# Optimization experiments

Measured on AMD Instinct MI355X. Metric: run time of the kernel, lower is better.

## Reference

```python
import jax, jax.numpy as jnp
import numpy as np

B, S, D, H, E, K = 4, 2048, 1024, 4096, 8, 2
CAP = 2048      # expert capacity (tokens)
ALPHA = 0.01    # load-balance loss coefficient


def setup_inputs() -> dict:
    key = jax.random.key(0)
    ks = jax.random.split(key, 8)
    def w(k, shape, fan_in):
        return jax.random.normal(k, shape, jnp.float32) * (fan_in ** -0.5)
    return {
        "input": jax.random.normal(ks[0], (B, S, D), jnp.float32),
        "rw": w(ks[1], (D, E), D), "rb": jnp.zeros((E,), jnp.float32),
        "w1": w(ks[2], (E, D, H), D), "b1": jnp.zeros((E, H), jnp.float32),
        "w2": w(ks[3], (E, H, D), H), "b2": jnp.zeros((E, D), jnp.float32),
        "ow1": w(ks[4], (D, H), D), "ob1": jnp.zeros((H,), jnp.float32),
        "ow2": w(ks[5], (H, D), H), "ob2": jnp.zeros((D,), jnp.float32),
    }


def _moe(x, rw, rb, w1, b1, w2, b2, ow1, ob1, ow2, ob2):
    Bx, Sx, Dx = x.shape
    N = Bx * Sx
    xf = x.reshape(N, Dx)

    # --- router: softmax -> top-k -> renormalize ---
    scores = jax.nn.softmax(xf @ rw + rb, axis=-1)          # [N,E]
    tw, ti = jax.lax.top_k(scores, K)                       # [N,K]
    tw = tw / tw.sum(-1, keepdims=True)
    onehot = jax.nn.one_hot(ti, E, dtype=xf.dtype)          # [N,K,E]
    w_ne = jnp.einsum('nk,nke->ne', tw, onehot)             # combine weight per (token, expert)
    mask = onehot.sum(1) > 0                                # [N,E]
    mi = mask.astype(jnp.int32)

    # exclusive rank of each token within its expert's queue (token order, as torch nonzero())
    rank = jnp.cumsum(mi, axis=0) - mi                      # [N,E]
    within = mask & (rank < CAP)
    over = mask & (rank >= CAP)

    # --- dispatch within-capacity tokens into [E, CAP] slots (sentinel = N) ---
    tok = jnp.broadcast_to(jnp.arange(N, dtype=jnp.int32)[:, None], (N, E))
    eid = jnp.broadcast_to(jnp.arange(E, dtype=jnp.int32)[None, :], (N, E))
    slot = jnp.where(within, rank, CAP)                     # non-assigned -> pad column
    buf = jnp.full((E, CAP + 1), N, dtype=jnp.int32)
    buf = buf.at[eid.reshape(-1), slot.reshape(-1)].set(tok.reshape(-1))
    buf = buf[:, :CAP]                                      # [E,CAP]

    xpad = jnp.concatenate([xf, jnp.zeros((1, Dx), xf.dtype)], axis=0)
    xd = xpad[buf]                                          # [E,CAP,D]

    # --- grouped expert FFN (Linear -> relu -> Linear) ---
    h = jax.nn.relu(jnp.einsum('ecd,edh->ech', xd, w1) + b1[:, None, :])
    y = jnp.einsum('ech,ehd->ecd', h, w2) + b2[:, None, :]  # [E,CAP,D]

    # combine weights gathered per slot; pad slots get weight 0
    wpad = jnp.concatenate([w_ne, jnp.zeros((1, E), w_ne.dtype)], axis=0)
    wc = wpad[buf, jnp.arange(E, dtype=jnp.int32)[:, None]]  # [E,CAP]

    outpad = jnp.zeros((N + 1, Dx), xf.dtype)
    outpad = outpad.at[buf.reshape(-1)].add((wc[..., None] * y).reshape(-1, Dx))
    out = outpad[:N]

    # --- overflow tokens -> shared overflow FFN (computed densely, masked by weight) ---
    w_of = (w_ne * over.astype(w_ne.dtype)).sum(-1)          # [N]
    yo = jax.nn.relu(xf @ ow1 + ob1) @ ow2 + ob2             # [N,D]
    out = out + w_of[:, None] * yo

    # --- aux load-balance loss (detached in torch via .item()) ---
    num = mi.sum(0)                                          # [E]
    cnt = jnp.minimum(num, CAP)
    f = cnt.astype(xf.dtype) / N
    p = (w_ne * within.astype(w_ne.dtype)).sum(0) / jnp.maximum(cnt, 1).astype(xf.dtype)
    aux = ALPHA * E * jnp.sum(f * p)
    return out.reshape(Bx, Sx, Dx), jax.lax.stop_gradient(aux)


def reference(input, rw, rb, w1, b1, w2, b2, ow1, ob1, ow2, ob2):
    return _moe(input, rw, rb, w1, b1, w2, b2, ow1, ob1, ow2, ob2)
```

## Files before the change

kernel.cpp:

```cpp
#include <hip/hip_runtime.h>
#include <cstdint>

typedef __attribute__((ext_vector_type(8))) short bf16x8;
typedef __attribute__((ext_vector_type(4))) float f32x4;

#define N_TOK    8192
#define DMODEL   1024
#define HDIM     4096
#define CAPACITY 2048

__device__ __forceinline__ unsigned short f2bf(float f) {
  unsigned u = __float_as_uint(f);
  u += 0x7FFFu + ((u >> 16) & 1u);
  return (unsigned short)(u >> 16);
}

__device__ __forceinline__ void gl_lds16(const unsigned short* g, unsigned short* l) {
  __builtin_amdgcn_global_load_lds(
      (const __attribute__((address_space(1))) void*)g,
      (__attribute__((address_space(3))) void*)l, 16, 0, 0);
}

__global__ void cvtx_kernel(const float* __restrict__ x, unsigned short* __restrict__ xb) {
  long i0 = ((long)blockIdx.x * 256 + threadIdx.x) * 16;
#pragma unroll
  for (int ii = 0; ii < 4; ii++) {
    float4 v = *(const float4*)(x + i0 + ii * 4);
    ushort4 u;
    u.x = f2bf(v.x); u.y = f2bf(v.y); u.z = f2bf(v.z); u.w = f2bf(v.w);
    *(ushort4*)(xb + i0 + ii * 4) = u;
  }
}

__global__ void router_kernel(const float* __restrict__ x, const float* __restrict__ rw,
                              const float* __restrict__ rb, int4* __restrict__ recs) {
  int wave = threadIdx.x >> 6;
  int lane = threadIdx.x & 63;
  int tok = blockIdx.x * 4 + wave;
  const float* xr = x + (long)tok * DMODEL;
  float s[8];
#pragma unroll
  for (int e = 0; e < 8; e++) s[e] = 0.f;
  for (int ii = 0; ii < DMODEL / 64; ii++) {
    int k = lane + 64 * ii;
    float xv = xr[k];
    const float* wr = rw + k * 8;
    float4 a = *(const float4*)wr;
    float4 b = *(const float4*)(wr + 4);
    s[0] += xv * a.x; s[1] += xv * a.y; s[2] += xv * a.z; s[3] += xv * a.w;
    s[4] += xv * b.x; s[5] += xv * b.y; s[6] += xv * b.z; s[7] += xv * b.w;
  }
#pragma unroll
  for (int m = 1; m < 64; m <<= 1) {
#pragma unroll
    for (int e = 0; e < 8; e++) s[e] += __shfl_xor(s[e], m);
  }
  if (lane == 0) {
#pragma unroll
    for (int e = 0; e < 8; e++) s[e] += rb[e];
    int b0 = 0; float v0 = s[0];
#pragma unroll
    for (int e = 1; e < 8; e++) if (s[e] > v0) { v0 = s[e]; b0 = e; }
    int b1 = -1; float v1 = 0.f;
#pragma unroll
    for (int e = 0; e < 8; e++) {
      if (e == b0) continue;
      if (b1 < 0 || s[e] > v1) { v1 = s[e]; b1 = e; }
    }
    float t0 = 1.f / (1.f + expf(v1 - v0));
    float t1 = 1.f - t0;
    recs[tok] = make_int4(b0, b1, __float_as_int(t0), __float_as_int(t1));
  }
}

__device__ __forceinline__ int bump16(uint4& v, int e) {
  unsigned sh = (e & 1) ? 16u : 0u;
  unsigned inc = 1u << sh;
  unsigned old;
  switch (e >> 1) {
    case 0: old = v.x; v.x += inc; break;
    case 1: old = v.y; v.y += inc; break;
    case 2: old = v.z; v.z += inc; break;
    default: old = v.w; v.w += inc; break;
  }
  return (int)((old >> sh) & 0xFFFFu);
}

__device__ __forceinline__ unsigned field16(uint4 v, int e) {
  unsigned w;
  switch (e >> 1) { case 0: w = v.x; break; case 1: w = v.y; break; case 2: w = v.z; break; default: w = v.w; break; }
  return (w >> ((e & 1) ? 16 : 0)) & 0xFFFFu;
}

__global__ void assign_kernel(const int4* __restrict__ recs, int* __restrict__ buf,
                              float* __restrict__ wc, int* __restrict__ cnt,
                              float* __restrict__ auxOut) {
  __shared__ uint4 sc[1024];
  __shared__ unsigned sco[1024];
  __shared__ float pnum[8];
  int tid = threadIdx.x;
  if (tid < 8) pnum[tid] = 0.f;
  int4 rc[8];
#pragma unroll
  for (int i = 0; i < 8; i++) {
    rc[i] = recs[tid * 8 + i];
    rc[i].x &= 7; rc[i].y &= 7;
  }
  uint4 c; c.x = c.y = c.z = c.w = 0u;
#pragma unroll
  for (int i = 0; i < 8; i++) { bump16(c, rc[i].x); bump16(c, rc[i].y); }
  sc[tid] = c;
  __syncthreads();
  for (int off = 1; off < 1024; off <<= 1) {
    uint4 v; v.x = v.y = v.z = v.w = 0u;
    if (tid >= off) v = sc[tid - off];
    __syncthreads();
    sc[tid].x += v.x; sc[tid].y += v.y; sc[tid].z += v.z; sc[tid].w += v.w;
    __syncthreads();
  }
  uint4 base; base.x = base.y = base.z = base.w = 0u;
  if (tid > 0) base = sc[tid - 1];
  uint4 totals = sc[1023];

  uint4 run = base;
  float wof[8];
  unsigned oc = 0;
#pragma unroll
  for (int i = 0; i < 8; i++) {
    int tk = tid * 8 + i;
    int e0 = rc[i].x, e1 = rc[i].y;
    float w0 = __int_as_float(rc[i].z);
    float w1 = __int_as_float(rc[i].w);
    float w = 0.f;
    int r0 = bump16(run, e0);
    if (r0 < CAPACITY) {
      buf[e0 * CAPACITY + r0] = tk;
      wc[e0 * CAPACITY + r0] = w0;
      atomicAdd(&pnum[e0], w0);
    } else w += w0;
    int r1 = bump16(run, e1);
    if (r1 < CAPACITY) {
      buf[e1 * CAPACITY + r1] = tk;
      wc[e1 * CAPACITY + r1] = w1;
      atomicAdd(&pnum[e1], w1);
    } else w += w1;
    wof[i] = w;
    if (w > 0.f) oc++;
  }
  sco[tid] = oc;
  __syncthreads();
  for (int off = 1; off < 1024; off <<= 1) {
    unsigned v = (tid >= off) ? sco[tid - off] : 0u;
    __syncthreads();
    sco[tid] += v;
    __syncthreads();
  }
  unsigned ob = (tid > 0) ? sco[tid - 1] : 0u;
  unsigned Ot = sco[1023];
#pragma unroll
  for (int i = 0; i < 8; i++) {
    if (wof[i] > 0.f) {
      unsigned slot = ob++;
      int ve = 8 + (int)(slot >> 11);
      buf[ve * CAPACITY + (int)(slot & 2047)] = tid * 8 + i;
      wc[ve * CAPACITY + (int)(slot & 2047)] = wof[i];
    }
  }
  __syncthreads();
  if (tid == 0) {
    float aux = 0.f;
#pragma unroll
    for (int e = 0; e < 8; e++) {
      int tot = (int)field16(totals, e);
      int c2 = tot < CAPACITY ? tot : CAPACITY;
      cnt[e] = c2;
      float f = (float)c2 / (float)N_TOK;
      float p = pnum[e] / (float)(c2 > 1 ? c2 : 1);
      aux += f * p;
    }
#pragma unroll
    for (int i = 0; i < 4; i++) {
      int c2 = (int)Ot - i * CAPACITY;
      c2 = c2 < 0 ? 0 : (c2 > CAPACITY ? CAPACITY : c2);
      cnt[8 + i] = c2;
    }
    auxOut[0] = 0.01f * 8.f * aux;
  }
}

__global__ __launch_bounds__(256) void transpose_all(
    const float* __restrict__ w1, const float* __restrict__ w2,
    const float* __restrict__ ow1, const float* __restrict__ ow2,
    unsigned short* __restrict__ wt1, unsigned short* __restrict__ wt2,
    long slotStride, int pairBase) {
  int pair = pairBase + blockIdx.x / 2048;
  int t = blockIdx.x & 2047;
  long srcOff = (long)pair * DMODEL * HDIM;
  long dstOff = (long)(blockIdx.x / 2048) * slotStride;
  const float* in; unsigned short* out; int R, C;
  if (t < 1024) {
    in = (pair < 8) ? w1 + srcOff : ow1;
    out = wt1 + dstOff;
    R = DMODEL; C = HDIM;
  } else {
    in = (pair < 8) ? w2 + srcOff : ow2;
    out = wt2 + dstOff;
    R = HDIM; C = DMODEL;
    t -= 1024;
  }
  int tr = t / (C >> 6);
  int tc = t % (C >> 6);
  int r0 = tr << 6, c0 = tc << 6;
  __shared__ float tl[64][65];
  int row = threadIdx.x >> 4, cg = threadIdx.x & 15;
#pragma unroll
  for (int i = 0; i < 4; i++) {
    int r = row + 16 * i;
    float4 v = *(const float4*)(in + (long)(r0 + r) * C + c0 + cg * 4);
    tl[r][cg * 4 + 0] = v.x; tl[r][cg * 4 + 1] = v.y;
    tl[r][cg * 4 + 2] = v.z; tl[r][cg * 4 + 3] = v.w;
  }
  __syncthreads();
#pragma unroll
  for (int i = 0; i < 4; i++) {
    int oc = row + 16 * i;
    ushort4 o;
    o.x = f2bf(tl[cg * 4 + 0][oc]);
    o.y = f2bf(tl[cg * 4 + 1][oc]);
    o.z = f2bf(tl[cg * 4 + 2][oc]);
    o.w = f2bf(tl[cg * 4 + 3][oc]);
    *(ushort4*)(out + (long)(c0 + oc) * R + r0 + cg * 4) = o;
  }
}


#define STAGE_A(Ab, kk)                                             \
  { _Pragma("unroll") for (int s = 0; s < 4; s++)                   \
      gl_lds16(asrc[s] + (kk), &(Ab)[wave * 2048 + s * 512]); }
#define STAGE_B(Bb, kk)                                             \
  { _Pragma("unroll") for (int s = 0; s < 4; s++)                   \
      gl_lds16(bsrc[s] + (kk), &(Bb)[wave * 2048 + s * 512]); }

#define R_A_FRAGS(dst, Abuf, ks)                                               \
  { _Pragma("unroll") for (int mi = 0; mi < 8; mi++) {                         \
      int r = mo + mi * 16 + l15;                                              \
      dst[mi] = *(const bf16x8*)&(Abuf)[r * 64 + ((((ks) * 4 + hi) ^ (r & 7)) << 3)]; \
    } }
#define R_B_FRAGS(dst, Bbuf, ks)                                               \
  { _Pragma("unroll") for (int ni = 0; ni < 4; ni++) {                         \
      int r = no + ni * 16 + l15;                                              \
      dst[ni] = *(const bf16x8*)&(Bbuf)[r * 64 + ((((ks) * 4 + hi) ^ (r & 7)) << 3)]; \
    } }

#define MFMA32(fa, fb)                                                         \
  { __builtin_amdgcn_s_setprio(1);                                             \
    _Pragma("unroll") for (int mi = 0; mi < 8; mi++)                           \
      _Pragma("unroll") for (int ni = 0; ni < 4; ni++)                         \
        acc[mi][ni] = __builtin_amdgcn_mfma_f32_16x16x32_bf16(fa[mi], fb[ni], acc[mi][ni], 0, 0, 0); \
    __builtin_amdgcn_s_setprio(0); }

#define K_PIPELINE(NT)                                              \
  do {                                                              \
    STAGE_A(As[0], 0); STAGE_B(Bs[0], 0);                           \
    STAGE_A(As[1], 64); STAGE_B(Bs[1], 64);                         \
    for (int t = 0; t < (NT); t++) {                                \
      unsigned short* Ac = As[t & 1];                               \
      unsigned short* Bc = Bs[t & 1];                               \
      if (t + 1 < (NT)) { asm volatile("s_waitcnt vmcnt(8)"); }     \
      else              { asm volatile("s_waitcnt vmcnt(0)"); }     \
      __builtin_amdgcn_sched_barrier(0);                            \
      __builtin_amdgcn_s_barrier();                                 \
      __builtin_amdgcn_sched_barrier(0);                            \
      bf16x8 fa0[8], fa1[8], fb0[4], fb1[4];                        \
      R_A_FRAGS(fa0, Ac, 0);                                        \
      R_A_FRAGS(fa1, Ac, 1);                                        \
      R_B_FRAGS(fb0, Bc, 0);                                        \
      __builtin_amdgcn_s_barrier();                                 \
      __builtin_amdgcn_sched_barrier(0);                            \
      if (t + 2 < (NT)) STAGE_A(Ac, (t + 2) * 64);                  \
      MFMA32(fa0, fb0);                                             \
      R_B_FRAGS(fb1, Bc, 1);                                        \
      __builtin_amdgcn_s_barrier();                                 \
      __builtin_amdgcn_sched_barrier(0);                            \
      if (t + 2 < (NT)) STAGE_B(Bc, (t + 2) * 64);                  \
      MFMA32(fa1, fb1);                                             \
    }                                                               \
  } while (0)

__global__ __launch_bounds__(512, 2) void gemm1_kernel(
    const unsigned short* __restrict__ xb, const int* __restrict__ buf,
    const int* __restrict__ cnt, const unsigned short* __restrict__ wt1, long wtStride,
    const float* __restrict__ b1, const float* __restrict__ ob1,
    unsigned short* __restrict__ h, long hStride, int eBase,
    const unsigned short* __restrict__ zp) {
  int q = gridDim.x >> 3;
  int bx = blockIdx.x;
  int id = (bx & 7) * q + (bx >> 3);
  int e = eBase + id / 128;
  int rem = id % 128;
  int mb = rem >> 4, nb = rem & 15;
  int m0 = mb * 256, n0 = nb * 256;
  if (m0 >= cnt[e]) return;
  const int* bufe = buf + e * CAPACITY;
  int slot = e < 8 ? e : 8;
  const unsigned short* wte = wt1 + (long)slot * wtStride;
  const float* bias = (e < 8) ? b1 + (long)e * HDIM : ob1;
  unsigned short* he = h + (long)e * hStride;

  __shared__ unsigned short As[2][256 * 64];
  __shared__ unsigned short Bs[2][256 * 64];

  int tid = threadIdx.x;
  int wave = tid >> 6, lane = tid & 63;
  int l15 = lane & 15, hi = lane >> 4;
  int wr = wave >> 2, wcv = wave & 3;
  int mo = wr * 128, no = wcv * 64;

  int rlo = lane >> 3;
  int cg = (lane & 7) ^ rlo;
  const unsigned short* asrc[4];
  const unsigned short* bsrc[4];
#pragma unroll
  for (int s = 0; s < 4; s++) {
    int r = wave * 32 + s * 8 + rlo;
    int tok = bufe[m0 + r];
    asrc[s] = ((unsigned)tok < (unsigned)N_TOK) ? (xb + (long)tok * DMODEL + cg * 8)
                                                : (zp + cg * 8);
    bsrc[s] = wte + (long)(n0 + r) * DMODEL + cg * 8;
  }

  f32x4 zero4 = {0.f, 0.f, 0.f, 0.f};
  f32x4 acc[8][4];
#pragma unroll
  for (int mi = 0; mi < 8; mi++)
#pragma unroll
    for (int ni = 0; ni < 4; ni++) acc[mi][ni] = zero4;

  K_PIPELINE(DMODEL / 64);

#pragma unroll
  for (int ni = 0; ni < 4; ni++) {
    int col = n0 + no + ni * 16 + l15;
    float bv = bias[col];
#pragma unroll
    for (int mi = 0; mi < 8; mi++) {
#pragma unroll
      for (int j = 0; j < 4; j++) {
        int mr = m0 + mo + mi * 16 + hi * 4 + j;
        float val = acc[mi][ni][j] + bv;
        val = val > 0.f ? val : 0.f;
        he[(long)mr * HDIM + col] = f2bf(val);
      }
    }
  }
}

__global__ __launch_bounds__(512, 2) void gemm2_kernel(
    const unsigned short* __restrict__ h, long hStride,
    const unsigned short* __restrict__ wt2, long wtStride,
    const float* __restrict__ b2, const float* __restrict__ ob2,
    const int* __restrict__ buf, const float* __restrict__ wc,
    const int* __restrict__ cnt, float* __restrict__ out,
    int eBase, int per, int klen) {
  int q = gridDim.x >> 3;
  int bx = blockIdx.x;
  int id = (bx & 7) * q + (bx >> 3);
  int e = eBase + id / per;
  int rem = id % per;
  int tile = rem & 31;
  int kc = rem >> 5;
  int mb = tile >> 2, nb = tile & 3;
  int m0 = mb * 256, n0 = nb * 256;
  if (m0 >= cnt[e]) return;
  const int* bufe = buf + e * CAPACITY;
  const float* wce = wc + e * CAPACITY;
  int slot = e < 8 ? e : 8;
  const unsigned short* wte = wt2 + (long)slot * wtStride;
  const float* bias = (e < 8) ? b2 + (long)e * DMODEL : ob2;
  const unsigned short* he = h + (long)e * hStride;
  int kbase = kc * klen;

  __shared__ unsigned short As[2][256 * 64];
  __shared__ unsigned short Bs[2][256 * 64];

  int tid = threadIdx.x;
  int wave = tid >> 6, lane = tid & 63;
  int l15 = lane & 15, hi = lane >> 4;
  int wr = wave >> 2, wcv = wave & 3;
  int mo = wr * 128, no = wcv * 64;

  int rlo = lane >> 3;
  int cg = (lane & 7) ^ rlo;
  const unsigned short* asrc[4];
  const unsigned short* bsrc[4];
#pragma unroll
  for (int s = 0; s < 4; s++) {
    int r = wave * 32 + s * 8 + rlo;
    asrc[s] = he + (long)(m0 + r) * HDIM + kbase + cg * 8;
    bsrc[s] = wte + (long)(n0 + r) * HDIM + kbase + cg * 8;
  }

  f32x4 zero4 = {0.f, 0.f, 0.f, 0.f};
  f32x4 acc[8][4];
#pragma unroll
  for (int mi = 0; mi < 8; mi++)
#pragma unroll
    for (int ni = 0; ni < 4; ni++) acc[mi][ni] = zero4;

  K_PIPELINE(klen / 64);

  float bcol[4];
#pragma unroll
  for (int ni = 0; ni < 4; ni++)
    bcol[ni] = (kc == 0) ? bias[n0 + no + ni * 16 + l15] : 0.f;
#pragma unroll
  for (int mi = 0; mi < 8; mi++) {
#pragma unroll
    for (int j = 0; j < 4; j++) {
      int m = m0 + mo + mi * 16 + hi * 4 + j;
      int t = bufe[m];
      if ((unsigned)t >= (unsigned)N_TOK) continue;
      float wv = wce[m];
      float* orow = out + (long)t * DMODEL;
#pragma unroll
      for (int ni = 0; ni < 4; ni++) {
        int col = n0 + no + ni * 16 + l15;
        float val = wv * (acc[mi][ni][j] + bcol[ni]);
        atomicAdd(orow + col, val);
      }
    }
  }
}

extern "C" void kernel_launch(void* const* d_in, const int* in_sizes, int n_in,
                              void* d_out, int out_size, void* d_ws, size_t ws_size,
                              hipStream_t stream) {
  const float* x   = (const float*)d_in[0];
  const float* rw  = (const float*)d_in[1];
  const float* rb  = (const float*)d_in[2];
  const float* w1  = (const float*)d_in[3];
  const float* b1  = (const float*)d_in[4];
  const float* w2  = (const float*)d_in[5];
  const float* b2  = (const float*)d_in[6];
  const float* ow1 = (const float*)d_in[7];
  const float* ob1 = (const float*)d_in[8];
  const float* ow2 = (const float*)d_in[9];
  const float* ob2 = (const float*)d_in[10];
  float* out = (float*)d_out;

  const long WSLOT = (long)DMODEL * HDIM;
  const long HSLOT = (long)CAPACITY * HDIM;

  bool fused = ws_size >= 380ull * 1024 * 1024;

  char* ws = (char*)d_ws;
  int4* recs = (int4*)(ws);
  int*  buf  = (int*)(ws + 131072);
  float* wcp = (float*)(ws + 229376);
  int*  cnt  = (int*)(ws + 327680);
  unsigned short* zp = (unsigned short*)(ws + 331776);
  unsigned short* xb  = (unsigned short*)(ws + 1048576);
  unsigned short* wt1 = (unsigned short*)(ws + 17825792);
  unsigned short* wt2;
  unsigned short* h;
  if (fused) {
    wt2 = (unsigned short*)(ws + 93323264);
    h   = (unsigned short*)(ws + 168820736);
  } else {
    wt2 = (unsigned short*)(ws + 26214400);
    h   = (unsigned short*)(ws + 34603008);
  }

  hipMemsetAsync(d_out, 0, (size_t)out_size * sizeof(float), stream);
  hipMemsetAsync(buf, 0xFF, 12 * CAPACITY * sizeof(int), stream);
  hipMemsetAsync(wcp, 0, 12 * CAPACITY * sizeof(float), stream);
  hipMemsetAsync(zp, 0, 2048, stream);

  cvtx_kernel<<<2048, 256, 0, stream>>>(x, xb);
  router_kernel<<<2048, 256, 0, stream>>>(x, rw, rb, recs);
  assign_kernel<<<1, 1024, 0, stream>>>(recs, buf, wcp, cnt, out + (long)N_TOK * DMODEL);

  if (fused) {
    transpose_all<<<9 * 2048, 256, 0, stream>>>(w1, w2, ow1, ow2, wt1, wt2, WSLOT, 0);
    gemm1_kernel<<<12 * 128, 512, 0, stream>>>(xb, buf, cnt, wt1, WSLOT, b1, ob1, h, HSLOT, 0, zp);
    gemm2_kernel<<<12 * 64, 512, 0, stream>>>(h, HSLOT, wt2, WSLOT, b2, ob2, buf, wcp, cnt, out,
                                              0, 64, HDIM / 2);
  } else {
    for (int e = 0; e < 12; e++) {
      if (e <= 8)
        transpose_all<<<2048, 256, 0, stream>>>(w1, w2, ow1, ow2, wt1, wt2, 0, e);
      gemm1_kernel<<<128, 512, 0, stream>>>(xb, buf, cnt, wt1, 0, b1, ob1, h, 0, e, zp);
      gemm2_kernel<<<64, 512, 0, stream>>>(h, 0, wt2, 0, b2, ob2, buf, wcp, cnt, out,
                                           e, 64, HDIM / 2);
    }
  }
}
```

Baseline: 660.3 us.

## Replace atomic scatter-add in down-proj with bf16 partials plus per-token reduce

```diff
diff --git a/kernel.cpp b/kernel.cpp
--- a/kernel.cpp
+++ b/kernel.cpp
@@ -8,11 +8,15 @@
 #define DMODEL   1024
 #define HDIM     4096
 #define CAPACITY 2048
+#define YKC      (12L * CAPACITY * DMODEL)
 
 __device__ __forceinline__ unsigned short f2bf(float f) {
   unsigned u = __float_as_uint(f);
   u += 0x7FFFu + ((u >> 16) & 1u);
   return (unsigned short)(u >> 16);
+}
+__device__ __forceinline__ float bf2f(unsigned short s) {
+  return __uint_as_float((unsigned)s << 16);
 }
 
 __device__ __forceinline__ void gl_lds16(const unsigned short* g, unsigned short* l) {
@@ -94,7 +98,7 @@
 
 __global__ void assign_kernel(const int4* __restrict__ recs, int* __restrict__ buf,
                               float* __restrict__ wc, int* __restrict__ cnt,
-                              float* __restrict__ auxOut) {
+                              int* __restrict__ trec, float* __restrict__ auxOut) {
   __shared__ uint4 sc[1024];
   __shared__ unsigned sco[1024];
   __shared__ float pnum[8];
@@ -144,6 +148,12 @@
       wc[e1 * CAPACITY + r1] = w1;
       atomicAdd(&pnum[e1], w1);
     } else w += w1;
+    trec[tk * 8 + 0] = (r0 < CAPACITY) ? (e0 * CAPACITY + r0) : -1;
+    trec[tk * 8 + 1] = (r1 < CAPACITY) ? (e1 * CAPACITY + r1) : -1;
+    trec[tk * 8 + 2] = -1;
+    trec[tk * 8 + 4] = rc[i].z;
+    trec[tk * 8 + 5] = rc[i].w;
+    trec[tk * 8 + 6] = 0;
     wof[i] = w;
     if (w > 0.f) oc++;
   }
@@ -162,8 +172,11 @@
     if (wof[i] > 0.f) {
       unsigned slot = ob++;
       int ve = 8 + (int)(slot >> 11);
-      buf[ve * CAPACITY + (int)(slot & 2047)] = tid * 8 + i;
+      int tk = tid * 8 + i;
+      buf[ve * CAPACITY + (int)(slot & 2047)] = tk;
       wc[ve * CAPACITY + (int)(slot & 2047)] = wof[i];
+      trec[tk * 8 + 2] = ve * CAPACITY + (int)(slot & 2047);
+      trec[tk * 8 + 6] = __float_as_int(wof[i]);
     }
   }
   __syncthreads();
@@ -287,6 +300,34 @@
     }                                                               \
   } while (0)
 
+#define EPILOGUE(VALEXPR, DSTPTR, DSTSTRIDE)                                   \
+  do {                                                                         \
+    __syncthreads();                                                           \
+    unsigned short* EP = &As[0][0];                                            \
+    for (int p = 0; p < 2; p++) {                                              \
+      if (wr == p) {                                                           \
+        _Pragma("unroll") for (int mi = 0; mi < 8; mi++) {                     \
+          _Pragma("unroll") for (int ni = 0; ni < 4; ni++) {                   \
+            int col = no + ni * 16 + l15;                                      \
+            _Pragma("unroll") for (int j = 0; j < 4; j++) {                    \
+              int row = mi * 16 + hi * 4 + j;                                  \
+              float v = (VALEXPR);                                             \
+              EP[row * 256 + (col ^ ((row & 7) << 3))] = f2bf(v);              \
+            }                                                                  \
+          }                                                                    \
+        }                                                                      \
+      }                                                                        \
+      __syncthreads();                                                         \
+      _Pragma("unroll") for (int k = 0; k < 8; k++) {                          \
+        int c = tid + 512 * k;                                                 \
+        int row = c >> 5, cc = c & 31;                                         \
+        uint4 v = *(const uint4*)&EP[row * 256 + ((cc ^ (row & 7)) << 3)];     \
+        *(uint4*)&(DSTPTR)[(long)(m0 + p * 128 + row) * (DSTSTRIDE) + n0 + cc * 8] = v; \
+      }                                                                        \
+      __syncthreads();                                                         \
+    }                                                                          \
+  } while (0)
+
 __global__ __launch_bounds__(512, 2) void gemm1_kernel(
     const unsigned short* __restrict__ xb, const int* __restrict__ buf,
     const int* __restrict__ cnt, const unsigned short* __restrict__ wt1, long wtStride,
@@ -338,24 +379,104 @@
 
   K_PIPELINE(DMODEL / 64);
 
-#pragma unroll
-  for (int ni = 0; ni < 4; ni++) {
-    int col = n0 + no + ni * 16 + l15;
-    float bv = bias[col];
-#pragma unroll
-    for (int mi = 0; mi < 8; mi++) {
-#pragma unroll
-      for (int j = 0; j < 4; j++) {
-        int mr = m0 + mo + mi * 16 + hi * 4 + j;
-        float val = acc[mi][ni][j] + bv;
-        val = val > 0.f ? val : 0.f;
-        he[(long)mr * HDIM + col] = f2bf(val);
-      }
-    }
-  }
+  EPILOGUE(fmaxf(acc[mi][ni][j] + bias[n0 + col], 0.f), he, HDIM);
 }
 
 __global__ __launch_bounds__(512, 2) void gemm2_kernel(
+    const unsigned short* __restrict__ h, long hStride,
+    const unsigned short* __restrict__ wt2, long wtStride,
+    const float* __restrict__ b2, const float* __restrict__ ob2,
+    const int* __restrict__ cnt, unsigned short* __restrict__ y,
+    int eBase, int per, int klen) {
+  int q = gridDim.x >> 3;
+  int bx = blockIdx.x;
+  int id = (bx & 7) * q + (bx >> 3);
+  int e = eBase + id / per;
+  int rem = id % per;
+  int tile = rem & 31;
+  int kc = rem >> 5;
+  int mb = tile >> 2, nb = tile & 3;
+  int m0 = mb * 256, n0 = nb * 256;
+  if (m0 >= cnt[e]) return;
+  int slot = e < 8 ? e : 8;
+  const unsigned short* wte = wt2 + (long)slot * wtStride;
+  const float* bias = (e < 8) ? b2 + (long)e * DMODEL : ob2;
+  const unsigned short* he = h + (long)e * hStride;
+  int kbase = kc * klen;
+  unsigned short* yb = y + (long)kc * YKC + (long)e * CAPACITY * DMODEL;
+
+  __shared__ unsigned short As[2][256 * 64];
+  __shared__ unsigned short Bs[2][256 * 64];
+
+  int tid = threadIdx.x;
+  int wave = tid >> 6, lane = tid & 63;
+  int l15 = lane & 15, hi = lane >> 4;
+  int wr = wave >> 2, wcv = wave & 3;
+  int mo = wr * 128, no = wcv * 64;
+
+  int rlo = lane >> 3;
+  int cg = (lane & 7) ^ rlo;
+  const unsigned short* asrc[4];
+  const unsigned short* bsrc[4];
+#pragma unroll
+  for (int s = 0; s < 4; s++) {
+    int r = wave * 32 + s * 8 + rlo;
+    asrc[s] = he + (long)(m0 + r) * HDIM + kbase + cg * 8;
+    bsrc[s] = wte + (long)(n0 + r) * HDIM + kbase + cg * 8;
+  }
+
+  f32x4 zero4 = {0.f, 0.f, 0.f, 0.f};
+  f32x4 acc[8][4];
+#pragma unroll
+  for (int mi = 0; mi < 8; mi++)
+#pragma unroll
+    for (int ni = 0; ni < 4; ni++) acc[mi][ni] = zero4;
+
+  K_PIPELINE(klen / 64);
+
+  EPILOGUE(acc[mi][ni][j] + (kc == 0 ? bias[n0 + col] : 0.f), yb, DMODEL);
+}
+
+__global__ __launch_bounds__(256) void reduce_kernel(
+    const unsigned short* __restrict__ y, const int* __restrict__ trec,
+    float* __restrict__ out) {
+  int tid = threadIdx.x;
+  int tok = blockIdx.x * 2 + (tid >> 7);
+  int l = tid & 127;
+  const int* r = trec + tok * 8;
+  int i0 = r[0], i1 = r[1], i2 = r[2];
+  float w0 = __int_as_float(r[4]);
+  float w1 = __int_as_float(r[5]);
+  float w2 = __int_as_float(r[6]);
+  long col = (long)l * 8;
+  float a[8];
+#pragma unroll
+  for (int k = 0; k < 8; k++) a[k] = 0.f;
+
+#define YADD(idx, w)                                                        \
+  if ((idx) >= 0) {                                                         \
+    const unsigned short* p0 = y + (long)(idx)*DMODEL + col;                \
+    const unsigned short* p1 = p0 + YKC;                                    \
+    uint4 u = *(const uint4*)p0;                                            \
+    uint4 v = *(const uint4*)p1;                                            \
+    const unsigned short* us = (const unsigned short*)&u;                   \
+    const unsigned short* vs = (const unsigned short*)&v;                   \
+    _Pragma("unroll") for (int k = 0; k < 8; k++)                           \
+      a[k] += (w) * (bf2f(us[k]) + bf2f(vs[k]));                            \
+  }
+  YADD(i0, w0);
+  YADD(i1, w1);
+  YADD(i2, w2);
+#undef YADD
+
+  float4 o0 = make_float4(a[0], a[1], a[2], a[3]);
+  float4 o1 = make_float4(a[4], a[5], a[6], a[7]);
+  float* dst = out + (long)tok * DMODEL + col;
+  *(float4*)dst = o0;
+  *(float4*)(dst + 4) = o1;
+}
+
+__global__ __launch_bounds__(512, 2) void gemm2_atomic(
     const unsigned short* __restrict__ h, long hStride,
     const unsigned short* __restrict__ wt2, long wtStride,
     const float* __restrict__ b2, const float* __restrict__ ob2,
@@ -451,46 +572,52 @@
   const long WSLOT = (long)DMODEL * HDIM;
   const long HSLOT = (long)CAPACITY * HDIM;
 
-  bool fused = ws_size >= 380ull * 1024 * 1024;
+  bool fused = ws_size >= 480ull * 1024 * 1024;
 
   char* ws = (char*)d_ws;
-  int4* recs = (int4*)(ws);
-  int*  buf  = (int*)(ws + 131072);
-  float* wcp = (float*)(ws + 229376);
-  int*  cnt  = (int*)(ws + 327680);
-  unsigned short* zp = (unsigned short*)(ws + 331776);
+  int4* recs  = (int4*)(ws);
+  int*  buf   = (int*)(ws + 131072);
+  float* wcp  = (float*)(ws + 229376);
+  int*  cnt   = (int*)(ws + 327680);
+  int*  trec  = (int*)(ws + 327744);
+  unsigned short* zp  = (unsigned short*)(ws + 655360);
   unsigned short* xb  = (unsigned short*)(ws + 1048576);
   unsigned short* wt1 = (unsigned short*)(ws + 17825792);
   unsigned short* wt2;
   unsigned short* h;
+  unsigned short* y = nullptr;
   if (fused) {
     wt2 = (unsigned short*)(ws + 93323264);
     h   = (unsigned short*)(ws + 168820736);
+    y   = (unsigned short*)(ws + 370147328);
   } else {
     wt2 = (unsigned short*)(ws + 26214400);
     h   = (unsigned short*)(ws + 34603008);
   }
 
-  hipMemsetAsync(d_out, 0, (size_t)out_size * sizeof(float), stream);
   hipMemsetAsync(buf, 0xFF, 12 * CAPACITY * sizeof(int), stream);
-  hipMemsetAsync(wcp, 0, 12 * CAPACITY * sizeof(float), stream);
   hipMemsetAsync(zp, 0, 2048, stream);
 
   cvtx_kernel<<<2048, 256, 0, stream>>>(x, xb);
   router_kernel<<<2048, 256, 0, stream>>>(x, rw, rb, recs);
-  assign_kernel<<<1, 1024, 0, stream>>>(recs, buf, wcp, cnt, out + (long)N_TOK * DMODEL);
+  assign_kernel<<<1, 1024, 0, stream>>>(recs, buf, wcp, cnt, trec,
+                                        out + (long)N_TOK * DMODEL);
 
   if (fused) {
     transpose_all<<<9 * 2048, 256, 0, stream>>>(w1, w2, ow1, ow2, wt1, wt2, WSLOT, 0);
-    gemm1_kernel<<<12 * 128, 512, 0, stream>>>(xb, buf, cnt, wt1, WSLOT, b1, ob1, h, HSLOT, 0, zp);
-    gemm2_kernel<<<12 * 64, 512, 0, stream>>>(h, HSLOT, wt2, WSLOT, b2, ob2, buf, wcp, cnt, out,
+    gemm1_kernel<<<12 * 128, 512, 0, stream>>>(xb, buf, cnt, wt1, WSLOT, b1, ob1,
+                                               h, HSLOT, 0, zp);
+    gemm2_kernel<<<12 * 64, 512, 0, stream>>>(h, HSLOT, wt2, WSLOT, b2, ob2, cnt, y,
                                               0, 64, HDIM / 2);
+    reduce_kernel<<<N_TOK / 2, 256, 0, stream>>>(y, trec, out);
   } else {
+    hipMemsetAsync(out, 0, (size_t)(N_TOK * DMODEL) * sizeof(float), stream);
+    hipMemsetAsync(wcp, 0, 12 * CAPACITY * sizeof(float), stream);
     for (int e = 0; e < 12; e++) {
       if (e <= 8)
         transpose_all<<<2048, 256, 0, stream>>>(w1, w2, ow1, ow2, wt1, wt2, 0, e);
       gemm1_kernel<<<128, 512, 0, stream>>>(xb, buf, cnt, wt1, 0, b1, ob1, h, 0, e, zp);
-      gemm2_kernel<<<64, 512, 0, stream>>>(h, 0, wt2, 0, b2, ob2, buf, wcp, cnt, out,
+      gemm2_atomic<<<64, 512, 0, stream>>>(h, 0, wt2, 0, b2, ob2, buf, wcp, cnt, out,
                                            e, 64, HDIM / 2);
     }
   }
```

Result: slower. 692.7 us (+4.9%).
